# Kernel tuning notes

Hardware: AMD Instinct MI355X
Metric: run time of the kernel (lower is better)

## Reference

```python
import jax, jax.numpy as jnp
import numpy as np

N_HEADS, INPUT_DIM, EMBED_DIM = 8, 128, 128
KEY_DIM = EMBED_DIM // N_HEADS  # val_dim = key_dim = 16
B, N = 8, 1024


def setup_inputs() -> dict:
    key = jax.random.key(0)
    ks = jax.random.split(key, 16)
    stdv_k = 1.0 / np.sqrt(KEY_DIM)
    stdv_e = 1.0 / np.sqrt(EMBED_DIM)

    def U(k, shape, s):
        return jax.random.uniform(k, shape, jnp.float32, -s, s)

    hdk = (N_HEADS, INPUT_DIM, KEY_DIM)
    hke = (N_HEADS, KEY_DIM, EMBED_DIM)
    return {
        "q_n": jax.random.normal(ks[0], (B, N, INPUT_DIM), jnp.float32),
        "q_c": jax.random.normal(ks[1], (B, N, INPUT_DIM), jnp.float32),
        "mask": jax.random.bernoulli(ks[2], 0.5, (B, N, N)),
        "W_query_n": U(ks[3], hdk, stdv_k),
        "W_key_nn": U(ks[4], hdk, stdv_k),
        "W_val_nn": U(ks[5], hdk, stdv_k),
        "W_key_c": U(ks[6], hdk, stdv_k),
        "W_val_c": U(ks[7], hdk, stdv_k),
        "W_query_c": U(ks[8], hdk, stdv_k),
        "W_key_n": U(ks[9], hdk, stdv_k),
        "W_val_n": U(ks[10], hdk, stdv_k),
        "W_out_node": U(ks[11], hke, stdv_e),
        "W_out_color": U(ks[12], hke, stdv_e),
    }


def reference(q_n, q_c, mask, W_query_n, W_key_nn, W_val_nn, W_key_c, W_val_c,
              W_query_c, W_key_n, W_val_n, W_out_node, W_out_color):
    norm = 1.0 / jnp.sqrt(jnp.asarray(KEY_DIM, q_n.dtype))
    neg_inf = jnp.asarray(-jnp.inf, q_n.dtype)

    def proj(x, W):  # (B,N,D), (H,D,K) -> (H,B,N,K)
        return jnp.einsum('bnd,hdk->hbnk', x, W)

    # --- color stream: q_c attends over nodes q_n ---
    Q_c = proj(q_c, W_query_c)
    K_n = proj(q_n, W_key_n)
    V_n = proj(q_n, W_val_n)
    attn_c = jax.nn.softmax(norm * jnp.einsum('hbqk,hbnk->hbqn', Q_c, K_n), axis=-1)
    heads_c = jnp.einsum('hbqn,hbnv->hbqv', attn_c, V_n)
    out_color = jnp.einsum('hbqv,hve->bqe', heads_c, W_out_color)

    # --- node stream: masked self-attention + attention over colors ---
    Q_n = proj(q_n, W_query_n)
    K_nn = proj(q_n, W_key_nn)
    V_nn = proj(q_n, W_val_nn)
    comp_nn = norm * jnp.einsum('hbqk,hbnk->hbqn', Q_n, K_nn)
    m = mask[None]  # (1,B,Q,N) broadcast over heads; True = not allowed
    comp_nn = jnp.where(m, neg_inf, comp_nn)
    attn_nn = jax.nn.softmax(comp_nn, axis=-1)
    attn_nn = jnp.where(m, jnp.asarray(0.0, q_n.dtype), attn_nn)
    heads_nn = jnp.einsum('hbqn,hbnv->hbqv', attn_nn, V_nn)

    K_nc = proj(q_c, W_key_c)
    V_nc = proj(q_c, W_val_c)
    attn_nc = jax.nn.softmax(norm * jnp.einsum('hbqk,hbnk->hbqn', Q_n, K_nc), axis=-1)
    heads_nc = jnp.einsum('hbqn,hbnv->hbqv', attn_nc, V_nc)

    heads = heads_nn + heads_nc
    out = jnp.einsum('hbqv,hve->bqe', heads, W_out_node)
    return (out, out_color)
```

## Files before the change

### kernel.cpp

```cpp
#include <hip/hip_runtime.h>
#include <stdint.h>

#define NH 8
#define NB 8
#define NN 1024
#define ND 128
#define NK 16
#define NF (NB*NN)
#define C2EXP 0.36067376022224085f
#define LSTR 136

typedef float f32x16 __attribute__((ext_vector_type(16)));
typedef short bf16x8 __attribute__((ext_vector_type(8)));

__device__ __forceinline__ float bf2f(uint16_t u){ return __uint_as_float(((uint32_t)u)<<16); }
__device__ __forceinline__ uint16_t f2bf(float f){
  uint32_t x = __float_as_uint(f);
  uint32_t r = (x + 0x7fffu + ((x>>16)&1u)) >> 16;
  return (uint16_t)r;
}
__device__ __forceinline__ float fast_exp2(float x){
#if __has_builtin(__builtin_amdgcn_exp2f)
  return __builtin_amdgcn_exp2f(x);
#else
  return exp2f(x);
#endif
}

__global__ __launch_bounds__(256) void pack_kernel(const int* __restrict__ mask,
                                                   uint32_t* __restrict__ packN){
  const int w = threadIdx.x >> 6, lane = threadIdx.x & 63;
  const int row = blockIdx.x*4 + w;
  const int* mp = mask + (size_t)row*NN;
  uint32_t* dst = packN + (size_t)row*32;
  for (int wq = 0; wq < 16; ++wq) {
    int v = mp[wq*64 + lane];
    unsigned long long bal = __ballot(v != 0);
    if (lane == 0) { dst[wq*2] = (uint32_t)bal; dst[wq*2+1] = (uint32_t)(bal>>32); }
  }
}

struct ProjArgs { const float* x[8]; const float* w[8]; };

__global__ __launch_bounds__(256) void proj_kernel(ProjArgs args, uint16_t* ws){
  __shared__ __align__(16) uint16_t WT[128*LSTR];
  __shared__ __align__(16) uint16_t S[128*LSTR];
  const int p = blockIdx.y;
  const int rb = blockIdx.x;
  const int tid = threadIdx.x;

  const float* wsrc = args.w[p];
  #pragma unroll 4
  for (int i = 0; i < 64; ++i) {
    int e = i*256 + tid;
    int h = e >> 11, d = (e >> 4) & 127, k = e & 15;
    WT[(h*16 + k)*LSTR + d] = f2bf(wsrc[e]);
  }
  __syncthreads();

  const int wave = tid >> 6, lane = tid & 63;
  const int l5 = lane >> 5, lm = lane & 31;
  const int r0 = rb*128 + wave*32;
  const float* xrow = args.x[p] + (size_t)(r0 + lm)*ND + l5*8;

  bf16x8 afr[8];
  #pragma unroll
  for (int kt = 0; kt < 8; ++kt) {
    float4 f0 = *(const float4*)(xrow + kt*16);
    float4 f1 = *(const float4*)(xrow + kt*16 + 4);
    bf16x8 a;
    a[0]=f2bf(f0.x); a[1]=f2bf(f0.y); a[2]=f2bf(f0.z); a[3]=f2bf(f0.w);
    a[4]=f2bf(f1.x); a[5]=f2bf(f1.y); a[6]=f2bf(f1.z); a[7]=f2bf(f1.w);
    afr[kt] = a;
  }

  const bool tr = (p==2)|(p==5)|(p==7);
  const float qsc = (p==0 || p==3) ? C2EXP : 1.0f;
  #pragma unroll
  for (int nt = 0; nt < 4; ++nt) {
    f32x16 acc;
    #pragma unroll
    for (int i = 0; i < 16; ++i) acc[i] = 0.f;
    #pragma unroll
    for (int kt = 0; kt < 8; ++kt) {
      bf16x8 b = *(const bf16x8*)(&WT[(nt*32 + lm)*LSTR + kt*16 + l5*8]);
      acc = __builtin_amdgcn_mfma_f32_32x32x16_bf16(afr[kt], b, acc, 0, 0, 0);
    }
    #pragma unroll
    for (int i = 0; i < 16; ++i) {
      int r = wave*32 + (i&3) + 8*(i>>2) + 4*l5;
      int c = nt*32 + lm;
      if (tr) S[c*LSTR + r] = f2bf(acc[i]*qsc);
      else    S[r*LSTR + c] = f2bf(acc[i]*qsc);
    }
  }
  __syncthreads();

  uint16_t* dst = ws + (size_t)p*((size_t)NH*NF*NK);
  if (!tr) {
    #pragma unroll
    for (int it = 0; it < 8; ++it) {
      int c = it*256 + tid;
      int row = c >> 4, cg = c & 15;
      bf16x8 v = *(const bf16x8*)(&S[row*LSTR + cg*8]);
      int h = cg >> 1, k8 = cg & 1;
      *(bf16x8*)(dst + ((size_t)h*NF + rb*128 + row)*NK + k8*8) = v;
    }
  } else {
    const int b = rb >> 3, nb = (rb & 7)*128;
    #pragma unroll
    for (int it = 0; it < 8; ++it) {
      int c = it*256 + tid;
      int col = c >> 4, ng = c & 15;
      bf16x8 v = *(const bf16x8*)(&S[col*LSTR + ng*8]);
      int h = col >> 4, k = col & 15;
      *(bf16x8*)(dst + ((size_t)(h*NB + b)*NK + k)*NN + nb + ng*8) = v;
    }
  }
}

template<bool MASKED>
__device__ __forceinline__ void attn_stream(
    const uint4* __restrict__ kbuf, bf16x8 aq,
    const uint16_t* __restrict__ VTb, const uint4* __restrict__ pmw4,
    int nh, int l5, int lm, f32x16& O, float& L)
{
  f32x16 Z;
  #pragma unroll
  for (int i = 0; i < 16; ++i) Z[i] = 0.f;
  for (int t4 = 0; t4 < 4; ++t4) {
    uint4 mq;
    if (MASKED) mq = pmw4[nh*4 + t4];
    #pragma unroll
    for (int j = 0; j < 4; ++j) {
      const int n0 = (nh*16 + t4*4 + j)*32;
      bf16x8 bk = *(const bf16x8*)(&kbuf[l5*1024 + n0 + lm]);
      f32x16 St = __builtin_amdgcn_mfma_f32_32x32x16_bf16(bk, aq, Z, 0, 0, 0);
      uint32_t mws = 0;
      if (MASKED) {
        uint32_t mw = (j==0) ? mq.x : (j==1) ? mq.y : (j==2) ? mq.z : mq.w;
        mws = mw >> (4*l5);
      }
      float p[16];
      #pragma unroll
      for (int i = 0; i < 16; ++i) {
        float pv = fast_exp2(St[i]);
        if (MASKED && ((mws >> ((i&3) + 8*(i>>2))) & 1u)) pv = 0.f;
        L += pv;
        p[i] = pv;
      }
      uint32_t o[8];
      #pragma unroll
      for (int k = 0; k < 8; ++k)
        o[k] = __builtin_amdgcn_perm(__float_as_uint(p[2*k+1]),
                                     __float_as_uint(p[2*k]), 0x07060302u);
      uint32_t s1 = l5 ? o[0] : o[2], s2 = l5 ? o[1] : o[3];
      uint32_t r1 = (uint32_t)__shfl_xor((int)s1, 32, 64);
      uint32_t r2 = (uint32_t)__shfl_xor((int)s2, 32, 64);
      uint32_t s3 = l5 ? o[4] : o[6], s4 = l5 ? o[5] : o[7];
      uint32_t r3 = (uint32_t)__shfl_xor((int)s3, 32, 64);
      uint32_t r4 = (uint32_t)__shfl_xor((int)s4, 32, 64);
      union { uint32_t u[4]; bf16x8 v; } B1, B2;
      B1.u[0] = l5 ? r1 : o[0];  B1.u[1] = l5 ? r2 : o[1];
      B1.u[2] = l5 ? o[2] : r1;  B1.u[3] = l5 ? o[3] : r2;
      B2.u[0] = l5 ? r3 : o[4];  B2.u[1] = l5 ? r4 : o[5];
      B2.u[2] = l5 ? o[6] : r3;  B2.u[3] = l5 ? o[7] : r4;
      bf16x8 av1, av2;
      #pragma unroll
      for (int i = 0; i < 8; ++i) { av1[i] = 0; av2[i] = 0; }
      if (lm < 16) {
        const uint16_t* vp = VTb + (size_t)lm*NN + n0 + l5*8;
        av1 = *(const bf16x8*)(vp);
        av2 = *(const bf16x8*)(vp + 16);
      }
      O = __builtin_amdgcn_mfma_f32_32x32x16_bf16(av1, B1.v, O, 0, 0, 0);
      O = __builtin_amdgcn_mfma_f32_32x32x16_bf16(av2, B2.v, O, 0, 0, 0);
    }
  }
}

template<bool DUAL>
__global__ __launch_bounds__(512, 4) void attn_kernel(
    const uint16_t* __restrict__ Q,
    const uint16_t* __restrict__ K1, const uint16_t* __restrict__ VT1,
    const uint16_t* __restrict__ K2, const uint16_t* __restrict__ VT2,
    const uint32_t* __restrict__ packN, uint16_t* __restrict__ outp)
{
  __shared__ uint4 kbuf[2048];
  __shared__ float comb[4*2*32*18];
  const int hb = blockIdx.y;
  const int h = hb >> 3, b = hb & 7;
  const size_t base = ((size_t)h*NF + (size_t)b*NN)*NK;
  const int tid = threadIdx.x;

  const uint4* k1 = (const uint4*)(K1 + base);
  for (int i = tid; i < 2048; i += 512)
    kbuf[(i & 1)*1024 + (i >> 1)] = k1[i];
  __syncthreads();

  const int wave = tid >> 6, lane = tid & 63;
  const int l5 = lane >> 5, lm = lane & 31;
  const int qt = wave & 3, nh = wave >> 2;
  const int q = blockIdx.x*128 + qt*32 + lm;

  const bf16x8 aq = *(const bf16x8*)(Q + base + (size_t)q*NK + l5*8);
  const uint4* pmw4 = DUAL ? (const uint4*)(packN + ((size_t)b*NN + q)*32)
                           : nullptr;

  f32x16 O1, O2;
  #pragma unroll
  for (int i = 0; i < 16; ++i) { O1[i] = 0.f; O2[i] = 0.f; }
  float L1 = 0.f, L2 = 0.f;

  attn_stream<DUAL>(kbuf, aq, VT1 + (size_t)hb*(NK*NN), pmw4, nh, l5, lm, O1, L1);
  if (DUAL) {
    __syncthreads();
    const uint4* k2 = (const uint4*)(K2 + base);
    for (int i = tid; i < 2048; i += 512)
      kbuf[(i & 1)*1024 + (i >> 1)] = k2[i];
    __syncthreads();
    attn_stream<false>(kbuf, aq, VT2 + (size_t)hb*(NK*NN), nullptr, nh, l5, lm, O2, L2);
  }

  L1 += __shfl_xor(L1, 32, 64);
  if (DUAL) L2 += __shfl_xor(L2, 32, 64);

  float* cw = comb + ((size_t)(qt*2 + l5)*32 + lm)*18;
  __syncthreads();
  if (nh == 1) {
    #pragma unroll
    for (int i = 0; i < 8; ++i) cw[i] = O1[i];
    if (DUAL) {
      #pragma unroll
      for (int i = 0; i < 8; ++i) cw[8+i] = O2[i];
    }
    cw[16] = L1; cw[17] = L2;
  }
  __syncthreads();
  if (nh == 0) {
    const float l1 = L1 + cw[16];
    const float i1 = (l1 > 0.f) ? 1.f/l1 : 0.f;
    float i2 = 0.f;
    if (DUAL) { const float l2 = L2 + cw[17]; i2 = (l2 > 0.f) ? 1.f/l2 : 0.f; }
    uint32_t w[4];
    #pragma unroll
    for (int k = 0; k < 4; ++k) {
      float va = (O1[2*k]   + cw[2*k])  *i1;
      float vb = (O1[2*k+1] + cw[2*k+1])*i1;
      if (DUAL) { va += (O2[2*k] + cw[8+2*k])*i2; vb += (O2[2*k+1] + cw[8+2*k+1])*i2; }
      w[k] = ((uint32_t)f2bf(vb) << 16) | f2bf(va);
    }
    uint16_t* hp = outp + ((size_t)b*NN + q)*128 + h*16 + l5*4;
    *(uint2*)(hp)     = make_uint2(w[0], w[1]);
    *(uint2*)(hp + 8) = make_uint2(w[2], w[3]);
  }
}

__global__ __launch_bounds__(256) void outproj_kernel(
    const uint16_t* __restrict__ hn, const uint16_t* __restrict__ hc,
    const float* __restrict__ wn, const float* __restrict__ wc,
    float* __restrict__ out)
{
  __shared__ __align__(16) uint16_t WT[128*LSTR];
  const int s = blockIdx.y;
  const int rb = blockIdx.x;
  const int tid = threadIdx.x;
  const float* wsrc = s ? wc : wn;
  #pragma unroll 4
  for (int i = 0; i < 64; ++i) {
    int e = i*256 + tid;
    int c = e >> 7, col = e & 127;
    WT[col*LSTR + c] = f2bf(wsrc[e]);
  }
  __syncthreads();

  const int wave = tid >> 6, lane = tid & 63;
  const int l5 = lane >> 5, lm = lane & 31;
  const int r0 = rb*128 + wave*32;
  const uint16_t* hp = (s ? hc : hn) + (size_t)(r0 + lm)*128 + l5*8;
  bf16x8 afr[8];
  #pragma unroll
  for (int kt = 0; kt < 8; ++kt) afr[kt] = *(const bf16x8*)(hp + kt*16);

  float* dst = out + (size_t)s*((size_t)NF*ND) + (size_t)r0*ND;
  #pragma unroll
  for (int nt = 0; nt < 4; ++nt) {
    f32x16 acc;
    #pragma unroll
    for (int i = 0; i < 16; ++i) acc[i] = 0.f;
    #pragma unroll
    for (int kt = 0; kt < 8; ++kt) {
      bf16x8 b = *(const bf16x8*)(&WT[(nt*32 + lm)*LSTR + kt*16 + l5*8]);
      acc = __builtin_amdgcn_mfma_f32_32x32x16_bf16(afr[kt], b, acc, 0, 0, 0);
    }
    #pragma unroll
    for (int i = 0; i < 16; ++i) {
      int r = (i&3) + 8*(i>>2) + 4*l5;
      dst[(size_t)r*ND + nt*32 + lm] = acc[i];
    }
  }
}

extern "C" void kernel_launch(void* const* d_in, const int* in_sizes, int n_in,
                              void* d_out, int out_size, void* d_ws, size_t ws_size,
                              hipStream_t stream)
{
  const float* q_n = (const float*)d_in[0];
  const float* q_c = (const float*)d_in[1];
  const int* mask = (const int*)d_in[2];
  const float* W[10];
  for (int i = 0; i < 10; ++i) W[i] = (const float*)d_in[3+i];

  uint16_t* ws16 = (uint16_t*)d_ws;
  const size_t PE = (size_t)NH*NF*NK;
  uint16_t* Qc   = ws16 + 0*PE;
  uint16_t* Kn   = ws16 + 1*PE;
  uint16_t* VTn  = ws16 + 2*PE;
  uint16_t* Qn   = ws16 + 3*PE;
  uint16_t* Knn  = ws16 + 4*PE;
  uint16_t* VTnn = ws16 + 5*PE;
  uint16_t* Knc  = ws16 + 6*PE;
  uint16_t* VTnc = ws16 + 7*PE;
  uint16_t* heads_node = ws16 + 8*PE;
  uint32_t* packN   = (uint32_t*)(ws16 + 9*PE);
  uint16_t* heads_c = ws16 + 9*PE;

  pack_kernel<<<2048, 256, 0, stream>>>(mask, packN);

  ProjArgs pa;
  pa.x[0]=q_c; pa.w[0]=W[5];
  pa.x[1]=q_n; pa.w[1]=W[6];
  pa.x[2]=q_n; pa.w[2]=W[7];
  pa.x[3]=q_n; pa.w[3]=W[0];
  pa.x[4]=q_n; pa.w[4]=W[1];
  pa.x[5]=q_n; pa.w[5]=W[2];
  pa.x[6]=q_c; pa.w[6]=W[3];
  pa.x[7]=q_c; pa.w[7]=W[4];
  proj_kernel<<<dim3(64, 8), 256, 0, stream>>>(pa, ws16);

  attn_kernel<true ><<<dim3(8,64), 512, 0, stream>>>(Qn, Knn, VTnn, Knc, VTnc,
                                                     packN, heads_node);
  attn_kernel<false><<<dim3(8,64), 512, 0, stream>>>(Qc, Kn, VTn, Kn, VTn,
                                                     nullptr, heads_c);

  outproj_kernel<<<dim3(64, 2), 256, 0, stream>>>(heads_node, heads_c, W[8], W[9],
                                                  (float*)d_out);
}
```

Before: 179.7 us.

## Merge attention launches, fold row-sum into MFMA, drop P shuffles, vectorize weight loads

The two attention launches are merged into one grid with a z dimension selecting the node or color stream. The softmax denominator is now computed by a row of ones in the V operand (lane 16), so a separate accumulator is no longer needed. The V^T layout is permuted during projection so that the P fragment can feed the second MFMA directly, removing the cross-half shuffles. Weight loads use float4, and the output projection launches twice as many blocks, each covering half the tile. The goal is to cut launch overhead, shuffle and VALU work, and raise occupancy, at the cost of more complex layout coupling between kernels.

```diff
diff --git a/kernel.cpp b/kernel.cpp
--- a/kernel.cpp
+++ b/kernel.cpp
@@ -13,7 +13,6 @@
 typedef float f32x16 __attribute__((ext_vector_type(16)));
 typedef short bf16x8 __attribute__((ext_vector_type(8)));
 
-__device__ __forceinline__ float bf2f(uint16_t u){ return __uint_as_float(((uint32_t)u)<<16); }
 __device__ __forceinline__ uint16_t f2bf(float f){
   uint32_t x = __float_as_uint(f);
   uint32_t r = (x + 0x7fffu + ((x>>16)&1u)) >> 16;
@@ -49,12 +48,16 @@
   const int rb = blockIdx.x;
   const int tid = threadIdx.x;
 
-  const float* wsrc = args.w[p];
-  #pragma unroll 4
-  for (int i = 0; i < 64; ++i) {
-    int e = i*256 + tid;
+  const float4* w4 = (const float4*)args.w[p];
+  #pragma unroll
+  for (int i = 0; i < 16; ++i) {
+    int e4 = i*256 + tid;
+    float4 f = w4[e4];
+    int e = e4*4;
     int h = e >> 11, d = (e >> 4) & 127, k = e & 15;
-    WT[(h*16 + k)*LSTR + d] = f2bf(wsrc[e]);
+    uint16_t* wr = &WT[(h*16 + k)*LSTR + d];
+    wr[0*LSTR] = f2bf(f.x); wr[1*LSTR] = f2bf(f.y);
+    wr[2*LSTR] = f2bf(f.z); wr[3*LSTR] = f2bf(f.w);
   }
   __syncthreads();
 
@@ -90,8 +93,13 @@
     for (int i = 0; i < 16; ++i) {
       int r = wave*32 + (i&3) + 8*(i>>2) + 4*l5;
       int c = nt*32 + lm;
-      if (tr) S[c*LSTR + r] = f2bf(acc[i]*qsc);
-      else    S[r*LSTR + c] = f2bf(acc[i]*qsc);
+      if (tr) {
+        int t2 = (r>>2)&3;
+        int rp = (t2==1 || t2==2) ? (r^12) : r;
+        S[c*LSTR + rp] = f2bf(acc[i]);
+      } else {
+        S[r*LSTR + c] = f2bf(acc[i]*qsc);
+      }
     }
   }
   __syncthreads();
@@ -123,7 +131,7 @@
 __device__ __forceinline__ void attn_stream(
     const uint4* __restrict__ kbuf, bf16x8 aq,
     const uint16_t* __restrict__ VTb, const uint4* __restrict__ pmw4,
-    int nh, int l5, int lm, f32x16& O, float& L)
+    int nh, int l5, int lm, f32x16& O)
 {
   f32x16 Z;
   #pragma unroll
@@ -146,25 +154,16 @@
       for (int i = 0; i < 16; ++i) {
         float pv = fast_exp2(St[i]);
         if (MASKED && ((mws >> ((i&3) + 8*(i>>2))) & 1u)) pv = 0.f;
-        L += pv;
         p[i] = pv;
       }
-      uint32_t o[8];
+      union { uint32_t u[4]; bf16x8 v; } B1, B2;
       #pragma unroll
-      for (int k = 0; k < 8; ++k)
-        o[k] = __builtin_amdgcn_perm(__float_as_uint(p[2*k+1]),
-                                     __float_as_uint(p[2*k]), 0x07060302u);
-      uint32_t s1 = l5 ? o[0] : o[2], s2 = l5 ? o[1] : o[3];
-      uint32_t r1 = (uint32_t)__shfl_xor((int)s1, 32, 64);
-      uint32_t r2 = (uint32_t)__shfl_xor((int)s2, 32, 64);
-      uint32_t s3 = l5 ? o[4] : o[6], s4 = l5 ? o[5] : o[7];
-      uint32_t r3 = (uint32_t)__shfl_xor((int)s3, 32, 64);
-      uint32_t r4 = (uint32_t)__shfl_xor((int)s4, 32, 64);
-      union { uint32_t u[4]; bf16x8 v; } B1, B2;
-      B1.u[0] = l5 ? r1 : o[0];  B1.u[1] = l5 ? r2 : o[1];
-      B1.u[2] = l5 ? o[2] : r1;  B1.u[3] = l5 ? o[3] : r2;
-      B2.u[0] = l5 ? r3 : o[4];  B2.u[1] = l5 ? r4 : o[5];
-      B2.u[2] = l5 ? o[6] : r3;  B2.u[3] = l5 ? o[7] : r4;
+      for (int k = 0; k < 4; ++k) {
+        B1.u[k] = __builtin_amdgcn_perm(__float_as_uint(p[2*k+1]),
+                                        __float_as_uint(p[2*k]),   0x07060302u);
+        B2.u[k] = __builtin_amdgcn_perm(__float_as_uint(p[2*k+9]),
+                                        __float_as_uint(p[2*k+8]), 0x07060302u);
+      }
       bf16x8 av1, av2;
       #pragma unroll
       for (int i = 0; i < 8; ++i) { av1[i] = 0; av2[i] = 0; }
@@ -172,6 +171,9 @@
         const uint16_t* vp = VTb + (size_t)lm*NN + n0 + l5*8;
         av1 = *(const bf16x8*)(vp);
         av2 = *(const bf16x8*)(vp + 16);
+      } else if (lm == 16) {
+        #pragma unroll
+        for (int i = 0; i < 8; ++i) { av1[i] = (short)0x3F80; av2[i] = (short)0x3F80; }
       }
       O = __builtin_amdgcn_mfma_f32_32x32x16_bf16(av1, B1.v, O, 0, 0, 0);
       O = __builtin_amdgcn_mfma_f32_32x32x16_bf16(av2, B2.v, O, 0, 0, 0);
@@ -179,15 +181,23 @@
   }
 }
 
-template<bool DUAL>
 __global__ __launch_bounds__(512, 4) void attn_kernel(
-    const uint16_t* __restrict__ Q,
-    const uint16_t* __restrict__ K1, const uint16_t* __restrict__ VT1,
-    const uint16_t* __restrict__ K2, const uint16_t* __restrict__ VT2,
-    const uint32_t* __restrict__ packN, uint16_t* __restrict__ outp)
+    const uint16_t* __restrict__ Qn_, const uint16_t* __restrict__ K1n,
+    const uint16_t* __restrict__ V1n, const uint16_t* __restrict__ K2n,
+    const uint16_t* __restrict__ V2n,
+    const uint16_t* __restrict__ Qc_, const uint16_t* __restrict__ K1c,
+    const uint16_t* __restrict__ V1c,
+    const uint32_t* __restrict__ packN,
+    uint16_t* __restrict__ hn_, uint16_t* __restrict__ hc_)
 {
   __shared__ uint4 kbuf[2048];
   __shared__ float comb[4*2*32*18];
+  const bool dual = (blockIdx.z == 0);
+  const uint16_t* Q   = dual ? Qn_ : Qc_;
+  const uint16_t* K1  = dual ? K1n : K1c;
+  const uint16_t* VT1 = dual ? V1n : V1c;
+  uint16_t* outp      = dual ? hn_ : hc_;
+
   const int hb = blockIdx.y;
   const int h = hb >> 3, b = hb & 7;
   const size_t base = ((size_t)h*NF + (size_t)b*NN)*NK;
@@ -204,33 +214,32 @@
   const int q = blockIdx.x*128 + qt*32 + lm;
 
   const bf16x8 aq = *(const bf16x8*)(Q + base + (size_t)q*NK + l5*8);
-  const uint4* pmw4 = DUAL ? (const uint4*)(packN + ((size_t)b*NN + q)*32)
-                           : nullptr;
+  const uint4* pmw4 = (const uint4*)(packN + ((size_t)b*NN + q)*32);
 
   f32x16 O1, O2;
   #pragma unroll
   for (int i = 0; i < 16; ++i) { O1[i] = 0.f; O2[i] = 0.f; }
-  float L1 = 0.f, L2 = 0.f;
-
-  attn_stream<DUAL>(kbuf, aq, VT1 + (size_t)hb*(NK*NN), pmw4, nh, l5, lm, O1, L1);
-  if (DUAL) {
+
+  if (dual) {
+    attn_stream<true>(kbuf, aq, V1n + (size_t)hb*(NK*NN), pmw4, nh, l5, lm, O1);
     __syncthreads();
-    const uint4* k2 = (const uint4*)(K2 + base);
+    const uint4* k2 = (const uint4*)(K2n + base);
     for (int i = tid; i < 2048; i += 512)
       kbuf[(i & 1)*1024 + (i >> 1)] = k2[i];
     __syncthreads();
-    attn_stream<false>(kbuf, aq, VT2 + (size_t)hb*(NK*NN), nullptr, nh, l5, lm, O2, L2);
-  }
-
-  L1 += __shfl_xor(L1, 32, 64);
-  if (DUAL) L2 += __shfl_xor(L2, 32, 64);
+    attn_stream<false>(kbuf, aq, V2n + (size_t)hb*(NK*NN), nullptr, nh, l5, lm, O2);
+  } else {
+    attn_stream<false>(kbuf, aq, V1c + (size_t)hb*(NK*NN), nullptr, nh, l5, lm, O1);
+  }
+
+  float L1 = O1[8] + __shfl_xor(O1[8], 32, 64);
+  float L2 = O2[8] + __shfl_xor(O2[8], 32, 64);
 
   float* cw = comb + ((size_t)(qt*2 + l5)*32 + lm)*18;
-  __syncthreads();
   if (nh == 1) {
     #pragma unroll
     for (int i = 0; i < 8; ++i) cw[i] = O1[i];
-    if (DUAL) {
+    if (dual) {
       #pragma unroll
       for (int i = 0; i < 8; ++i) cw[8+i] = O2[i];
     }
@@ -241,13 +250,13 @@
     const float l1 = L1 + cw[16];
     const float i1 = (l1 > 0.f) ? 1.f/l1 : 0.f;
     float i2 = 0.f;
-    if (DUAL) { const float l2 = L2 + cw[17]; i2 = (l2 > 0.f) ? 1.f/l2 : 0.f; }
+    if (dual) { const float l2 = L2 + cw[17]; i2 = (l2 > 0.f) ? 1.f/l2 : 0.f; }
     uint32_t w[4];
     #pragma unroll
     for (int k = 0; k < 4; ++k) {
       float va = (O1[2*k]   + cw[2*k])  *i1;
       float vb = (O1[2*k+1] + cw[2*k+1])*i1;
-      if (DUAL) { va += (O2[2*k] + cw[8+2*k])*i2; vb += (O2[2*k+1] + cw[8+2*k+1])*i2; }
+      if (dual) { va += (O2[2*k] + cw[8+2*k])*i2; vb += (O2[2*k+1] + cw[8+2*k+1])*i2; }
       w[k] = ((uint32_t)f2bf(vb) << 16) | f2bf(va);
     }
     uint16_t* hp = outp + ((size_t)b*NN + q)*128 + h*16 + l5*4;
@@ -266,17 +275,23 @@
   const int rb = blockIdx.x;
   const int tid = threadIdx.x;
   const float* wsrc = s ? wc : wn;
-  #pragma unroll 4
-  for (int i = 0; i < 64; ++i) {
-    int e = i*256 + tid;
+  const float4* w4 = (const float4*)wsrc;
+  #pragma unroll
+  for (int i = 0; i < 16; ++i) {
+    int e4 = i*256 + tid;
+    float4 f = w4[e4];
+    int e = e4*4;
     int c = e >> 7, col = e & 127;
-    WT[col*LSTR + c] = f2bf(wsrc[e]);
+    uint16_t* wr = &WT[col*LSTR + c];
+    wr[0*LSTR] = f2bf(f.x); wr[1*LSTR] = f2bf(f.y);
+    wr[2*LSTR] = f2bf(f.z); wr[3*LSTR] = f2bf(f.w);
   }
   __syncthreads();
 
   const int wave = tid >> 6, lane = tid & 63;
   const int l5 = lane >> 5, lm = lane & 31;
-  const int r0 = rb*128 + wave*32;
+  const int rt = wave & 1, nh2 = wave >> 1;
+  const int r0 = rb*64 + rt*32;
   const uint16_t* hp = (s ? hc : hn) + (size_t)(r0 + lm)*128 + l5*8;
   bf16x8 afr[8];
   #pragma unroll
@@ -284,7 +299,8 @@
 
   float* dst = out + (size_t)s*((size_t)NF*ND) + (size_t)r0*ND;
   #pragma unroll
-  for (int nt = 0; nt < 4; ++nt) {
+  for (int nt2 = 0; nt2 < 2; ++nt2) {
+    const int nt = nh2*2 + nt2;
     f32x16 acc;
     #pragma unroll
     for (int i = 0; i < 16; ++i) acc[i] = 0.f;
@@ -338,11 +354,10 @@
   pa.x[7]=q_c; pa.w[7]=W[4];
   proj_kernel<<<dim3(64, 8), 256, 0, stream>>>(pa, ws16);
 
-  attn_kernel<true ><<<dim3(8,64), 512, 0, stream>>>(Qn, Knn, VTnn, Knc, VTnc,
-                                                     packN, heads_node);
-  attn_kernel<false><<<dim3(8,64), 512, 0, stream>>>(Qc, Kn, VTn, Kn, VTn,
-                                                     nullptr, heads_c);
-
-  outproj_kernel<<<dim3(64, 2), 256, 0, stream>>>(heads_node, heads_c, W[8], W[9],
-                                                  (float*)d_out);
-}
+  attn_kernel<<<dim3(8, 64, 2), 512, 0, stream>>>(
+      Qn, Knn, VTnn, Knc, VTnc, Qc, Kn, VTn, packN,
+      heads_node, ws16 + 10*PE);
+
+  outproj_kernel<<<dim3(128, 2), 256, 0, stream>>>(heads_node, ws16 + 10*PE,
+                                                   W[8], W[9], (float*)d_out);
+}
```

Result: faster. 167.8 us (-6.7%).
